# Kernel optimization log

Measured on AMD Instinct MI355X. Metric: run time of the kernel, lower is better.

## Reference

```python
import jax, jax.numpy as jnp
import numpy as np

B, S, D_IN, E, H = 4, 2048, 768, 768, 12
HD = E // H                      # 64
WIN_PCT = 10                     # window_size init arg (percent of valid length)
MAX_LEN = 2048
MIN_WIN = 2
PAD = -1e9
TEMP = 1.0


def setup_inputs() -> dict:
    key = jax.random.key(0)
    k1, k2, k3 = jax.random.split(key, 3)
    return {
        "x": jax.random.normal(k1, (B, S, D_IN), dtype=jnp.float32),
        "src_key_padding_mask": jnp.zeros((B, S), dtype=jnp.int32),   # 0 = valid token
        "matrix_mask": jnp.zeros((B, S, S), dtype=jnp.float32),       # additive mask, 0 or PAD
        "qkv_w": jax.random.normal(k2, (3 * E, D_IN), dtype=jnp.float32) * 0.02,
        "qkv_b": jnp.zeros((3 * E,), dtype=jnp.float32),
        "o_w": jax.random.normal(k3, (E, E), dtype=jnp.float32) * 0.02,
        "o_b": jnp.zeros((E,), dtype=jnp.float32),
    }


def _sliding_window_mask(src_key_padding_mask, matrix_mask):
    # per-sample window size = ceil(valid_len * WIN_PCT / 100), clamped to >= MIN_WIN
    lens = (src_key_padding_mask == 0).sum(axis=1)                    # [B]
    clipped = jnp.minimum(lens, MAX_LEN).astype(jnp.float32)
    wsz = jnp.maximum(jnp.ceil(clipped * WIN_PCT / 100.0), MIN_WIN)   # [B] float ok for compare
    idx = jnp.arange(S)
    dist = jnp.abs(idx[None, :, None] - idx[None, None, :])           # [1,S,S]
    window_mask = dist > wsz[:, None, None]                           # [B,S,S] bool
    merged = window_mask | (matrix_mask == PAD)
    return jnp.where(merged, PAD, matrix_mask)                        # [B,S,S]


def reference(x, src_key_padding_mask, matrix_mask, qkv_w, qkv_b, o_w, o_b):
    mask = _sliding_window_mask(src_key_padding_mask, matrix_mask)    # [B,S,S]
    qkv = x @ qkv_w.T + qkv_b                                         # [B,S,3E]
    # torch: reshape(B,S,H,3*HD) then chunk along last dim
    qkv = qkv.reshape(B, S, H, 3 * HD).transpose(0, 2, 1, 3)          # [B,H,S,3*HD]
    q, k, v = jnp.split(qkv, 3, axis=-1)                              # each [B,H,S,HD]
    scale = 1.0 / np.sqrt(HD)
    logits = jnp.einsum("bhqd,bhkd->bhqk", q, k) * scale + mask[:, None]
    attn = jax.nn.softmax(logits / TEMP, axis=-1)                     # [B,H,S,S]
    values = jnp.einsum("bhqk,bhkd->bhqd", attn, v)                   # [B,H,S,HD]
    attn_mean = attn.mean(axis=1)                                     # [B,S,S]
    values = values.transpose(0, 2, 1, 3).reshape(B, S, E)            # [B,S,E]
    o = values @ o_w.T + o_b
    return (o, attn_mean)
```

## Files before the change

### kernel.cpp

```cpp
#include <hip/hip_runtime.h>

#define SEQ 2048
#define NB 4
#define DIN 768
#define EDIM 768
#define NH 12
#define QKVN 2304
#define SCALE 0.125f
#define PADV -1e9f
#define INV12 (0.0833333333f)
#define PSW 520

typedef unsigned short ushort_t;
typedef __attribute__((ext_vector_type(8))) short bf16x8;
typedef __attribute__((ext_vector_type(4))) float f32x4;

__device__ __forceinline__ float bf2f(ushort_t u) {
    union { unsigned int i; float f; } v; v.i = ((unsigned int)u) << 16; return v.f;
}
__device__ __forceinline__ ushort_t f2bf(float f) {
    union { float f; unsigned int i; } v; v.f = f;
    unsigned int r = (v.i + 0x7fffu + ((v.i >> 16) & 1u)) >> 16;
    return (ushort_t)r;
}
__device__ __forceinline__ void gl_lds16(const ushort_t* g, ushort_t* l) {
    __builtin_amdgcn_global_load_lds(
        (const __attribute__((address_space(1))) unsigned int*)(g),
        (__attribute__((address_space(3))) unsigned int*)(l),
        16, 0, 0);
}

__global__ void cvt3_kernel(const float* __restrict__ s0, int n0,
                            const float* __restrict__ s1, int n1,
                            const float* __restrict__ s2, int n2,
                            ushort_t* __restrict__ d0, ushort_t* __restrict__ d1,
                            ushort_t* __restrict__ d2) {
    int i = blockIdx.x * blockDim.x + threadIdx.x;
    const float* src; ushort_t* dst; int off;
    if (i < n0)               { src = s0; dst = d0; off = i; }
    else if (i < n0 + n1)     { src = s1; dst = d1; off = i - n0; }
    else if (i < n0 + n1 + n2){ src = s2; dst = d2; off = i - n0 - n1; }
    else return;
    float4 f = ((const float4*)src)[off];
    ushort4 u;
    u.x = f2bf(f.x); u.y = f2bf(f.y); u.z = f2bf(f.z); u.w = f2bf(f.w);
    ((ushort4*)dst)[off] = u;
}

template<int MODE>
__global__ __launch_bounds__(256) void mfma_gemm128(
    const ushort_t* __restrict__ A, const ushort_t* __restrict__ Bw,
    const float* __restrict__ bias, float* __restrict__ outf,
    ushort_t* __restrict__ qkh, ushort_t* __restrict__ vt, int N, int K)
{
    __shared__ __align__(16) ushort_t Al[128 * 64];
    __shared__ __align__(16) ushort_t Bl[128 * 64];
    const int tid  = threadIdx.x;
    const int w    = tid >> 6;
    const int l    = tid & 63;
    const int quad = l >> 4;
    const int lr   = l & 15;
    const int mw   = (w >> 1) * 64;
    const int nw   = (w & 1) * 64;
    const int bm   = blockIdx.y * 128;
    const int bn   = blockIdx.x * 128;
    const int srow = l >> 3;
    const int sg   = (l & 7) ^ srow;

    f32x4 acc[4][4];
    #pragma unroll
    for (int i = 0; i < 4; ++i)
        #pragma unroll
        for (int j = 0; j < 4; ++j)
            #pragma unroll
            for (int r = 0; r < 4; ++r) acc[i][j][r] = 0.f;

    const ushort_t* ga = A  + (size_t)(bm + w * 32 + srow) * K + sg * 8;
    const ushort_t* gb = Bw + (size_t)(bn + w * 32 + srow) * K + sg * 8;
    ushort_t* la = &Al[(w * 32) * 64];
    ushort_t* lb = &Bl[(w * 32) * 64];

    for (int k0 = 0; k0 < K; k0 += 64) {
        __syncthreads();
        #pragma unroll
        for (int i = 0; i < 4; ++i)
            gl_lds16(ga + (size_t)(i * 8) * K + k0, la + i * 8 * 64);
        #pragma unroll
        for (int i = 0; i < 4; ++i)
            gl_lds16(gb + (size_t)(i * 8) * K + k0, lb + i * 8 * 64);
        __syncthreads();
        #pragma unroll
        for (int s = 0; s < 2; ++s) {
            bf16x8 af[4], bf[4];
            #pragma unroll
            for (int t = 0; t < 4; ++t)
                af[t] = *(const bf16x8*)&Al[(mw + t * 16 + lr) * 64 + (((4 * s + quad) ^ (lr & 7)) * 8)];
            #pragma unroll
            for (int t = 0; t < 4; ++t)
                bf[t] = *(const bf16x8*)&Bl[(nw + t * 16 + lr) * 64 + (((4 * s + quad) ^ (lr & 7)) * 8)];
            #pragma unroll
            for (int mt = 0; mt < 4; ++mt)
                #pragma unroll
                for (int nt = 0; nt < 4; ++nt)
                    acc[mt][nt] = __builtin_amdgcn_mfma_f32_16x16x32_bf16(af[mt], bf[nt], acc[mt][nt], 0, 0, 0);
        }
    }

    #pragma unroll
    for (int nt = 0; nt < 4; ++nt) {
        const int gn = bn + nw + nt * 16 + lr;
        const float bv = bias[gn];
        const int hh  = gn / 192;
        const int rem = gn - hh * 192;
        #pragma unroll
        for (int mt = 0; mt < 4; ++mt) {
            const int gm0 = bm + mw + mt * 16 + quad * 4;
            if (MODE == 0) {
                #pragma unroll
                for (int r = 0; r < 4; ++r)
                    outf[(size_t)(gm0 + r) * N + gn] = acc[mt][nt][r] + bv;
            } else if (rem < 128) {
                const int bb  = gm0 >> 11;
                const int tok = gm0 & (SEQ - 1);
                #pragma unroll
                for (int r = 0; r < 4; ++r)
                    qkh[((size_t)(bb * NH + hh) * SEQ + tok + r) * 128 + rem] =
                        f2bf(acc[mt][nt][r] + bv);
            } else {
                const int bb  = gm0 >> 11;
                const int tok = gm0 & (SEQ - 1);
                ushort4 st;
                st.x = f2bf(acc[mt][nt][0] + bv);
                st.y = f2bf(acc[mt][nt][1] + bv);
                st.z = f2bf(acc[mt][nt][2] + bv);
                st.w = f2bf(acc[mt][nt][3] + bv);
                *(ushort4*)&vt[((size_t)(bb * NH + hh) * 64 + (rem - 128)) * SEQ + tok] = st;
            }
        }
    }
}

__global__ __launch_bounds__(512) void attn_kernel(
    const ushort_t* __restrict__ qkh,
    const ushort_t* __restrict__ vt,
    const float* __restrict__ mmask,
    const int* __restrict__ pad,
    ushort_t* __restrict__ values,
    float* __restrict__ attn_out)
{
    __shared__ __align__(16) ushort_t Ps[2][16 * PSW];
    __shared__ float lsump[2][4][16];
    __shared__ int s_cnt[8];
    __shared__ int s_flags[8];
    const int tid  = threadIdx.x;
    const int w    = tid >> 6;
    const int hg   = w >> 2;
    const int ww   = w & 3;
    const int lane = tid & 63;
    const int quad = lane >> 4;
    const int lr   = lane & 15;

    const int lin  = blockIdx.x;
    const int s    = lin & 1;
    const int b    = (lin >> 1) & 3;
    const int i16  = (lin >> 3) + 64 * s;
    const int iq0  = i16 * 16;

    {
        int4 pv = *(const int4*)&pad[b * SEQ + tid * 4];
        int c = (pv.x == 0) + (pv.y == 0) + (pv.z == 0) + (pv.w == 0);
        #pragma unroll
        for (int o = 32; o; o >>= 1) c += __shfl_down(c, o, 64);
        if (lane == 0) s_cnt[w] = c;
        if (tid < 8) s_flags[tid] = 0;
    }
    __syncthreads();
    int len = 0;
    #pragma unroll
    for (int k = 0; k < 8; ++k) len += s_cnt[k];
    if (len > 2048) len = 2048;
    int wsz = (int)ceilf((float)len * 10.0f / 100.0f);
    if (wsz < 2) wsz = 2;

    const int jlo  = max(0, iq0 - wsz);
    const int jhi  = min(SEQ - 1, iq0 + 15 + wsz);
    const int jt0  = jlo >> 6;
    const int nch  = (jhi >> 6) - jt0 + 1;
    const int jbase = jt0 << 6;
    const int span  = nch << 6;

    {
        const float* tp = mmask + ((size_t)b * SEQ + iq0) * SEQ + jbase;
        const int e = tid * 2, row = e >> 6, col = e & 63;
        for (int ci = 0; ci < nch; ++ci) {
            float2 v = *(const float2*)&tp[(size_t)row * SEQ + ci * 64 + col];
            if (__any(v.x != 0.f || v.y != 0.f)) {
                if (lane == 0) atomicOr(&s_flags[ci], 1);
            }
        }
    }

    const int arow = tid & 15;
    const int acg  = tid >> 4;
    float acc[16];
    #pragma unroll
    for (int k = 0; k < 16; ++k) acc[k] = 0.f;
    __syncthreads();

    const ushort_t* vhead = vt + (size_t)b * NH * 64 * SEQ;

    for (int hp = 0; hp < NH / 2; ++hp) {
        const int h = hp * 2 + hg;
        const ushort_t* hbase = qkh + (size_t)(b * NH + h) * SEQ * 128;
        const ushort_t* qbase = hbase + (size_t)(iq0 + lr) * 128;
        const bf16x8 qf0 = *(const bf16x8*)(qbase + quad * 8);
        const bf16x8 qf1 = *(const bf16x8*)(qbase + 32 + quad * 8);

        float ls[4] = {0.f, 0.f, 0.f, 0.f};
        #pragma unroll
        for (int cc = 0; cc < 2; ++cc) {
            const int ci = ww + cc * 4;
            if (ci < nch) {
                const int jc = jbase + ci * 64;
                f32x4 s4[4];
                #pragma unroll
                for (int t = 0; t < 4; ++t) {
                    const ushort_t* kr = hbase + (size_t)(jc + t * 16 + lr) * 128 + 64;
                    bf16x8 kf0 = *(const bf16x8*)(kr + quad * 8);
                    bf16x8 kf1 = *(const bf16x8*)(kr + 32 + quad * 8);
                    #pragma unroll
                    for (int r = 0; r < 4; ++r) s4[t][r] = 0.f;
                    s4[t] = __builtin_amdgcn_mfma_f32_16x16x32_bf16(qf0, kf0, s4[t], 0, 0, 0);
                    s4[t] = __builtin_amdgcn_mfma_f32_16x16x32_bf16(qf1, kf1, s4[t], 0, 0, 0);
                }
                const int anym = s_flags[ci];
                #pragma unroll
                for (int t = 0; t < 4; ++t) {
                    const int gj = jc + t * 16 + lr;
                    #pragma unroll
                    for (int r = 0; r < 4; ++r) {
                        const int gi = iq0 + quad * 4 + r;
                        float mm = 0.f;
                        if (anym) mm = mmask[((size_t)b * SEQ + gi) * SEQ + gj];
                        const int dist = gi > gj ? gi - gj : gj - gi;
                        const float p = (dist > wsz) ? 0.f : __expf(fmaf(s4[t][r], SCALE, mm));
                        ls[r] += p;
                        Ps[hg][(quad * 4 + r) * PSW + (ci * 64 + t * 16 + lr)] = f2bf(p);
                    }
                }
            }
        }
        #pragma unroll
        for (int r = 0; r < 4; ++r) {
            #pragma unroll
            for (int m = 8; m; m >>= 1) ls[r] += __shfl_xor(ls[r], m, 16);
        }
        if (lr == 0) {
            #pragma unroll
            for (int r = 0; r < 4; ++r) lsump[hg][ww][quad * 4 + r] = ls[r];
        }
        __syncthreads();

        if (acg * 16 < span) {
            const float l0 = lsump[0][0][arow] + lsump[0][1][arow] + lsump[0][2][arow] + lsump[0][3][arow];
            const float l1 = lsump[1][0][arow] + lsump[1][1][arow] + lsump[1][2][arow] + lsump[1][3][arow];
            const float sc0 = INV12 / l0;
            const float sc1 = INV12 / l1;
            const ushort_t* p0 = &Ps[0][arow * PSW + acg * 16];
            const ushort_t* p1 = &Ps[1][arow * PSW + acg * 16];
            #pragma unroll
            for (int k = 0; k < 4; ++k) {
                ushort4 u0 = *(const ushort4*)(p0 + k * 4);
                ushort4 u1 = *(const ushort4*)(p1 + k * 4);
                acc[k * 4 + 0] = fmaf(bf2f(u0.x), sc0, fmaf(bf2f(u1.x), sc1, acc[k * 4 + 0]));
                acc[k * 4 + 1] = fmaf(bf2f(u0.y), sc0, fmaf(bf2f(u1.y), sc1, acc[k * 4 + 1]));
                acc[k * 4 + 2] = fmaf(bf2f(u0.z), sc0, fmaf(bf2f(u1.z), sc1, acc[k * 4 + 2]));
                acc[k * 4 + 3] = fmaf(bf2f(u0.w), sc0, fmaf(bf2f(u1.w), sc1, acc[k * 4 + 3]));
            }
        }

        {
            f32x4 oacc;
            #pragma unroll
            for (int r = 0; r < 4; ++r) oacc[r] = 0.f;
            const ushort_t* vrow = vhead + (size_t)(h * 64 + ww * 16 + lr) * SEQ + jbase;
            for (int ci = 0; ci < nch; ++ci) {
                const int tok0 = ci * 64;
                #pragma unroll
                for (int s2 = 0; s2 < 2; ++s2) {
                    bf16x8 pa = *(const bf16x8*)&Ps[hg][lr * PSW + tok0 + s2 * 32 + quad * 8];
                    bf16x8 vf = *(const bf16x8*)(vrow + tok0 + s2 * 32 + quad * 8);
                    oacc = __builtin_amdgcn_mfma_f32_16x16x32_bf16(pa, vf, oacc, 0, 0, 0);
                }
            }
            float lr4[4];
            #pragma unroll
            for (int r = 0; r < 4; ++r)
                lr4[r] = lsump[hg][0][quad * 4 + r] + lsump[hg][1][quad * 4 + r] +
                         lsump[hg][2][quad * 4 + r] + lsump[hg][3][quad * 4 + r];
            #pragma unroll
            for (int r = 0; r < 4; ++r) {
                const int row = iq0 + quad * 4 + r;
                values[(size_t)(b * SEQ + row) * EDIM + h * 64 + ww * 16 + lr] =
                    f2bf(oacc[r] / lr4[r]);
            }
        }
        __syncthreads();
    }

    if (acg * 16 < span) {
        float* dst = attn_out + ((size_t)b * SEQ + iq0 + arow) * SEQ + jbase + acg * 16;
        #pragma unroll
        for (int k = 0; k < 4; ++k) {
            float4 v = { acc[k * 4 + 0], acc[k * 4 + 1], acc[k * 4 + 2], acc[k * 4 + 3] };
            *(float4*)(dst + k * 4) = v;
        }
    }
    {
        const int c4lo = jbase >> 2;
        const int c4hi = (jbase + span) >> 2;
        const float4 z = {0.f, 0.f, 0.f, 0.f};
        for (int f = tid; f < 16 * 512; f += 512) {
            const int i  = f >> 9;
            const int c4 = f & 511;
            if (c4 < c4lo || c4 >= c4hi)
                *(float4*)(attn_out + ((size_t)b * SEQ + iq0 + i) * SEQ + c4 * 4) = z;
        }
    }
}

extern "C" void kernel_launch(void* const* d_in, const int* in_sizes, int n_in,
                              void* d_out, int out_size, void* d_ws, size_t ws_size,
                              hipStream_t stream) {
    const float* x      = (const float*)d_in[0];
    const int*   pad    = (const int*)d_in[1];
    const float* mmask  = (const float*)d_in[2];
    const float* qkv_w  = (const float*)d_in[3];
    const float* qkv_b  = (const float*)d_in[4];
    const float* o_w    = (const float*)d_in[5];
    const float* o_b    = (const float*)d_in[6];

    float* out_o    = (float*)d_out;
    float* out_attn = out_o + (size_t)NB * SEQ * EDIM;

    ushort_t* qkh    = (ushort_t*)d_ws;
    ushort_t* vt     = qkh + (size_t)NB * NH * SEQ * 128;
    ushort_t* xb     = vt + (size_t)NB * NH * 64 * SEQ;
    ushort_t* values = xb;
    ushort_t* wqkvb  = xb + (size_t)NB * SEQ * DIN;
    ushort_t* wob    = wqkvb + (size_t)QKVN * DIN;

    const int nx = NB * SEQ * DIN / 4, nw1 = QKVN * DIN / 4, nw2 = EDIM * EDIM / 4;
    cvt3_kernel<<<(nx + nw1 + nw2 + 255) / 256, 256, 0, stream>>>(
        x, nx, qkv_w, nw1, o_w, nw2, xb, wqkvb, wob);

    mfma_gemm128<1><<<dim3(QKVN / 128, (NB * SEQ) / 128), 256, 0, stream>>>(
        xb, wqkvb, qkv_b, nullptr, qkh, vt, QKVN, DIN);

    attn_kernel<<<512, 512, 0, stream>>>(
        qkh, vt, mmask, pad, values, out_attn);

    mfma_gemm128<0><<<dim3(EDIM / 128, (NB * SEQ) / 128), 256, 0, stream>>>(
        values, wob, o_b, out_o, nullptr, nullptr, EDIM, EDIM);
}
```

Before: 328.9 us.

## Fuse output projection into attention kernel via LDS-staged values tile

Each attention block now keeps its 16x768 bf16 values tile in shared memory and multiplies it by the bf16 output weight inside the same kernel. Each wave computes 96 output columns, reading weights straight from global memory. This removes the separate output-projection GEMM launch and the global round trip of the values tensor. In exchange every block rereads the whole weight matrix from global or L2, about 1.2 MB per block across 512 blocks, and uses more LDS, which could lower occupancy.

After: 396.8 us. 1.21x slower.

```diff
diff --git a/kernel.cpp b/kernel.cpp
--- a/kernel.cpp
+++ b/kernel.cpp
@@ -10,6 +10,7 @@
 #define PADV -1e9f
 #define INV12 (0.0833333333f)
 #define PSW 520
+#define VSTR 776
 
 typedef unsigned short ushort_t;
 typedef __attribute__((ext_vector_type(8))) short bf16x8;
@@ -47,10 +48,9 @@
     ((ushort4*)dst)[off] = u;
 }
 
-template<int MODE>
 __global__ __launch_bounds__(256) void mfma_gemm128(
     const ushort_t* __restrict__ A, const ushort_t* __restrict__ Bw,
-    const float* __restrict__ bias, float* __restrict__ outf,
+    const float* __restrict__ bias,
     ushort_t* __restrict__ qkh, ushort_t* __restrict__ vt, int N, int K)
 {
     __shared__ __align__(16) ushort_t Al[128 * 64];
@@ -115,20 +115,14 @@
         #pragma unroll
         for (int mt = 0; mt < 4; ++mt) {
             const int gm0 = bm + mw + mt * 16 + quad * 4;
-            if (MODE == 0) {
-                #pragma unroll
-                for (int r = 0; r < 4; ++r)
-                    outf[(size_t)(gm0 + r) * N + gn] = acc[mt][nt][r] + bv;
-            } else if (rem < 128) {
-                const int bb  = gm0 >> 11;
-                const int tok = gm0 & (SEQ - 1);
+            const int bb  = gm0 >> 11;
+            const int tok = gm0 & (SEQ - 1);
+            if (rem < 128) {
                 #pragma unroll
                 for (int r = 0; r < 4; ++r)
                     qkh[((size_t)(bb * NH + hh) * SEQ + tok + r) * 128 + rem] =
                         f2bf(acc[mt][nt][r] + bv);
             } else {
-                const int bb  = gm0 >> 11;
-                const int tok = gm0 & (SEQ - 1);
                 ushort4 st;
                 st.x = f2bf(acc[mt][nt][0] + bv);
                 st.y = f2bf(acc[mt][nt][1] + bv);
@@ -145,10 +139,13 @@
     const ushort_t* __restrict__ vt,
     const float* __restrict__ mmask,
     const int* __restrict__ pad,
-    ushort_t* __restrict__ values,
+    const ushort_t* __restrict__ wob,
+    const float* __restrict__ o_b,
+    float* __restrict__ out_o,
     float* __restrict__ attn_out)
 {
     __shared__ __align__(16) ushort_t Ps[2][16 * PSW];
+    __shared__ __align__(16) ushort_t vals[16 * VSTR];
     __shared__ float lsump[2][4][16];
     __shared__ int s_cnt[8];
     __shared__ int s_flags[8];
@@ -299,13 +296,43 @@
                 lr4[r] = lsump[hg][0][quad * 4 + r] + lsump[hg][1][quad * 4 + r] +
                          lsump[hg][2][quad * 4 + r] + lsump[hg][3][quad * 4 + r];
             #pragma unroll
-            for (int r = 0; r < 4; ++r) {
-                const int row = iq0 + quad * 4 + r;
-                values[(size_t)(b * SEQ + row) * EDIM + h * 64 + ww * 16 + lr] =
+            for (int r = 0; r < 4; ++r)
+                vals[(quad * 4 + r) * VSTR + h * 64 + ww * 16 + lr] =
                     f2bf(oacc[r] / lr4[r]);
-            }
         }
         __syncthreads();
+    }
+
+    {
+        const int col0 = w * 96;
+        f32x4 oaccs[6];
+        #pragma unroll
+        for (int t = 0; t < 6; ++t)
+            #pragma unroll
+            for (int r = 0; r < 4; ++r) oaccs[t][r] = 0.f;
+        for (int qx = 0; qx < 4; ++qx) {
+            bf16x8 af[6];
+            #pragma unroll
+            for (int ks = 0; ks < 6; ++ks)
+                af[ks] = *(const bf16x8*)&vals[lr * VSTR + qx * 192 + ks * 32 + quad * 8];
+            #pragma unroll
+            for (int t = 0; t < 6; ++t) {
+                const ushort_t* bw = wob + (size_t)(col0 + t * 16 + lr) * EDIM + qx * 192 + quad * 8;
+                #pragma unroll
+                for (int ks = 0; ks < 6; ++ks) {
+                    bf16x8 bf = *(const bf16x8*)(bw + ks * 32);
+                    oaccs[t] = __builtin_amdgcn_mfma_f32_16x16x32_bf16(af[ks], bf, oaccs[t], 0, 0, 0);
+                }
+            }
+        }
+        #pragma unroll
+        for (int t = 0; t < 6; ++t) {
+            const float bv = o_b[col0 + t * 16 + lr];
+            #pragma unroll
+            for (int r = 0; r < 4; ++r)
+                out_o[(size_t)(b * SEQ + iq0 + quad * 4 + r) * EDIM + col0 + t * 16 + lr] =
+                    oaccs[t][r] + bv;
+        }
     }
 
     if (acg * 16 < span) {
@@ -346,7 +373,6 @@
     ushort_t* qkh    = (ushort_t*)d_ws;
     ushort_t* vt     = qkh + (size_t)NB * NH * SEQ * 128;
     ushort_t* xb     = vt + (size_t)NB * NH * 64 * SEQ;
-    ushort_t* values = xb;
     ushort_t* wqkvb  = xb + (size_t)NB * SEQ * DIN;
     ushort_t* wob    = wqkvb + (size_t)QKVN * DIN;
 
@@ -354,12 +380,9 @@
     cvt3_kernel<<<(nx + nw1 + nw2 + 255) / 256, 256, 0, stream>>>(
         x, nx, qkv_w, nw1, o_w, nw2, xb, wqkvb, wob);
 
-    mfma_gemm128<1><<<dim3(QKVN / 128, (NB * SEQ) / 128), 256, 0, stream>>>(
-        xb, wqkvb, qkv_b, nullptr, qkh, vt, QKVN, DIN);
+    mfma_gemm128<<<dim3(QKVN / 128, (NB * SEQ) / 128), 256, 0, stream>>>(
+        xb, wqkvb, qkv_b, qkh, vt, QKVN, DIN);
 
     attn_kernel<<<512, 512, 0, stream>>>(
-        qkh, vt, mmask, pad, values, out_attn);
-
-    mfma_gemm128<0><<<dim3(EDIM / 128, (NB * SEQ) / 128), 256, 0, stream>>>(
-        values, wob, o_b, out_o, nullptr, nullptr, EDIM, EDIM);
-}
+        qkh, vt, mmask, pad, wob, o_b, out_o, out_attn);
+}
```
